# Optimization experiments

Hardware: AMD Instinct MI355X
Metric: run time of the kernel (lower is better)

Reference implementation:

```python
import jax, jax.numpy as jnp
import numpy as np

S, B, I, H, L, D = 512, 64, 128, 256, 6, 2  # seq, batch, input, hidden, layers, directions


def setup_inputs() -> dict:
    key = jax.random.key(0)
    ks = jax.random.split(key, 7)
    stdv = 1.0 / np.sqrt(H)
    u = lambda k, shape: jax.random.uniform(k, shape, jnp.float32, -stdv, stdv)
    return {
        "x": jax.random.normal(ks[0], (S, B, I), jnp.float32),
        "h0": jax.random.normal(ks[1], (L * D, B, H), jnp.float32),
        "w_ih0": u(ks[2], (D, 3 * H, I)),            # layer 0 input weights
        "w_ih": u(ks[3], (L - 1, D, 3 * H, D * H)),  # layers 1.. input weights
        "w_hh": u(ks[4], (L, D, 3 * H, H)),
        "b_ih": u(ks[5], (L, D, 3 * H)),
        "b_hh": u(ks[6], (L, D, 3 * H)),
    }


def _gru_direction(gate_x, w_hh, b_hh, h0, reverse):
    # gate_x: (S, B, 3H) precomputed x @ W_ih.T + b_ih; scan the recurrence.
    def step(h, gx):
        gh = h @ w_hh.T + b_hh  # (B, 3H)
        x_r, x_z, x_n = jnp.split(gx, 3, axis=-1)
        h_r, h_z, h_n = jnp.split(gh, 3, axis=-1)
        r = jax.nn.sigmoid(x_r + h_r)
        z = jax.nn.sigmoid(x_z + h_z)
        n = jnp.tanh(x_n + r * h_n)
        h_new = (1.0 - z) * n + z * h
        return h_new, h_new

    h_last, ys = jax.lax.scan(step, h0, gate_x, reverse=reverse)
    return h_last, ys  # ys aligned with input time order even when reverse=True


def reference(x, h0, w_ih0, w_ih, w_hh, b_ih, b_hh):
    num_layers = w_hh.shape[0]
    inp = x  # (S, B, in_dim)
    h_n = []
    for layer in range(num_layers):
        outs = []
        for d in range(2):
            w = w_ih0[d] if layer == 0 else w_ih[layer - 1, d]
            # Single GEMM over the whole sequence for the input gates.
            gate_x = jnp.einsum('sbi,gi->sbg', inp, w) + b_ih[layer, d]
            h_last, ys = _gru_direction(
                gate_x, w_hh[layer, d], b_hh[layer, d],
                h0[layer * 2 + d], reverse=(d == 1))
            outs.append(ys)
            h_n.append(h_last)
        inp = jnp.concatenate(outs, axis=-1)  # (S, B, 2H)
    return jnp.stack(h_n)  # (L*2, B, H)
```

## Files before the change

kernel.cpp:

```cpp
#include <hip/hip_runtime.h>
#include <stdint.h>

#define S_LEN 512
#define NB    64
#define HID   256
#define G3    768
#define SB    32768
#define NLAYER 6

typedef short bf16x8 __attribute__((ext_vector_type(8)));
typedef short bf16x4 __attribute__((ext_vector_type(4)));
typedef float floatx4 __attribute__((ext_vector_type(4)));
typedef unsigned short u16;
typedef unsigned int   u32;

__device__ __forceinline__ float bf2f(u16 v) {
  u32 u = ((u32)v) << 16;
  return __builtin_bit_cast(float, u);
}
__device__ __forceinline__ u16 f2bf(float f) {
  u32 u = __builtin_bit_cast(u32, f);
  u = (u + 0x7FFFu + ((u >> 16) & 1u)) >> 16;
  return (u16)u;
}
__device__ __forceinline__ float fsigmoid(float x) {
  return __builtin_amdgcn_rcpf(1.0f + __expf(-x));
}
__device__ __forceinline__ float ftanh(float x) {
  return 1.0f - 2.0f * __builtin_amdgcn_rcpf(1.0f + __expf(x + x));
}

__device__ __forceinline__ void lds_barrier() {
  asm volatile("s_waitcnt lgkmcnt(0)\n\ts_barrier" ::: "memory");
}

__global__ void detect_fp32(const u16* __restrict__ x, int n, int* flag) {
  __shared__ int tot;
  if (threadIdx.x == 0) tot = 0;
  __syncthreads();
  int c = 0;
  for (int i = threadIdx.x; i < n; i += blockDim.x) {
    u16 v = x[i];
    if (((v >> 7) & 0xFF) == 0xFF) ++c;
  }
  atomicAdd(&tot, c);
  __syncthreads();
  if (threadIdx.x == 0) *flag = (tot > 64) ? 1 : 0;
}

__global__ void cvt(const void* __restrict__ src, u16* __restrict__ dst,
                    int n, const int* __restrict__ flag) {
  const int stride = gridDim.x * blockDim.x;
  const bool isf32 = (*flag != 0);
  for (int i = blockIdx.x * blockDim.x + threadIdx.x; i < n; i += stride) {
    if (isf32) dst[i] = f2bf(((const float*)src)[i]);
    else       dst[i] = ((const u16*)src)[i];
  }
}

__global__ void prep_bias(const u16* __restrict__ bih, const u16* __restrict__ bhh,
                          float* __restrict__ bc, int n) {
  int i = blockIdx.x * blockDim.x + threadIdx.x;
  if (i >= n) return;
  int col = i % G3;
  float v = bf2f(bih[i]);
  if (col < 512) v += bf2f(bhh[i]);
  bc[i] = v;
}

__global__ void write_out(const float* __restrict__ hNs, void* __restrict__ out,
                          int n, const int* __restrict__ flag) {
  int i = blockIdx.x * blockDim.x + threadIdx.x;
  if (i >= n) return;
  if (*flag) ((float*)out)[i] = hNs[i];
  else       ((u16*)out)[i]   = f2bf(hNs[i]);
}

__global__ __launch_bounds__(256)
void gate_gemm(const u16* __restrict__ A, const u16* __restrict__ W,
               const float* __restrict__ bias, u16* __restrict__ outg, int K) {
  const int m0  = blockIdx.x * 128;
  const int n0  = blockIdx.y * 128;
  const int dir = blockIdx.z;
  W    += (size_t)dir * G3 * K;
  bias += (size_t)dir * G3;
  outg += (size_t)dir * (size_t)SB * G3;

  __shared__ __align__(16) u16 lA[8192];
  __shared__ __align__(16) u16 lB[8192];

  const int tid  = threadIdx.x;
  const int lane = tid & 63;
  const int wv   = tid >> 6;
  const int wm   = wv & 1, wn = wv >> 1;
  const int l15  = lane & 15, quad = lane >> 4;

  floatx4 acc[4][4] = {};

  for (int k0 = 0; k0 < K; k0 += 64) {
    bf16x8 ra[4], rb[4];
#pragma unroll
    for (int i = 0; i < 4; ++i) {
      int c   = i * 256 + tid;
      int row = c >> 3;
      int kc  = (c & 7) ^ (row & 7);
      ra[i] = *(const bf16x8*)(A + (size_t)(m0 + row) * K + (k0 + kc * 8));
      rb[i] = *(const bf16x8*)(W + (size_t)(n0 + row) * K + (k0 + kc * 8));
    }
    __syncthreads();
#pragma unroll
    for (int i = 0; i < 4; ++i) {
      *(bf16x8*)(lA + (size_t)(i * 256 + tid) * 8) = ra[i];
      *(bf16x8*)(lB + (size_t)(i * 256 + tid) * 8) = rb[i];
    }
    __syncthreads();

#pragma unroll
    for (int kt = 0; kt < 2; ++kt) {
      bf16x8 af[4], bfr[4];
#pragma unroll
      for (int mt = 0; mt < 4; ++mt) {
        int row = wm * 64 + mt * 16 + l15;
        int ch  = row * 8 + ((kt * 4 + quad) ^ (row & 7));
        af[mt] = *(const bf16x8*)(lA + ch * 8);
      }
#pragma unroll
      for (int nt = 0; nt < 4; ++nt) {
        int row = wn * 64 + nt * 16 + l15;
        int ch  = row * 8 + ((kt * 4 + quad) ^ (row & 7));
        bfr[nt] = *(const bf16x8*)(lB + ch * 8);
      }
#pragma unroll
      for (int mt = 0; mt < 4; ++mt)
#pragma unroll
        for (int nt = 0; nt < 4; ++nt)
          acc[mt][nt] = __builtin_amdgcn_mfma_f32_16x16x32_bf16(
              af[mt], bfr[nt], acc[mt][nt], 0, 0, 0);
    }
  }

  const int sIdx = (m0 >> 6) + wm;
#pragma unroll
  for (int nt = 0; nt < 4; ++nt) {
    int n    = n0 + wn * 64 + nt * 16 + l15;
    int g    = n >> 8, jc = n & 255;
    float bv = bias[n];
#pragma unroll
    for (int mt = 0; mt < 4; ++mt) {
      bf16x4 pk;
#pragma unroll
      for (int r = 0; r < 4; ++r) pk[r] = (short)f2bf(acc[mt][nt][r] + bv);
      *(bf16x4*)(outg + ((((size_t)mt * 512 + sIdx) * 256 + jc) * 3 + g) * 16 +
                 quad * 4) = pk;
    }
  }
}

__global__ __launch_bounds__(512)
__attribute__((amdgpu_waves_per_eu(2, 2)))
void gru_scan(const u16* __restrict__ gateX,
              const u16* __restrict__ Whh,
              const u16* __restrict__ Bhh,
              const u16* __restrict__ H0,
              u16* __restrict__ layerOut,
              float* __restrict__ hNs,
              int layer) {
  const int dir = blockIdx.x & 1;
  const int bg  = blockIdx.x >> 1;
  const int tid = threadIdx.x;
  const int lane = tid & 63;
  const int wv   = tid >> 6;
  const int l15  = lane & 15, quad = lane >> 4;

  __shared__ __align__(16) u16 wnL[65536];
  __shared__ __align__(16) u16 hb2[2][4096];

  const u16* Wd = Whh + (size_t)dir * G3 * HID;

#pragma unroll
  for (int i = 0; i < 16; ++i) {
    int c    = i * 512 + tid;
    int n    = c >> 5;
    int slot = c & 31;
    bf16x8 v = *(const bf16x8*)(Wd + (size_t)(512 + n) * HID + slot * 8);
    *(bf16x8*)(wnL + n * 256 + ((slot ^ (n & 7)) * 8)) = v;
  }

  bf16x8 wrz[8][2][2];
#pragma unroll
  for (int g = 0; g < 2; ++g)
#pragma unroll
    for (int nt = 0; nt < 2; ++nt) {
      int n = g * 256 + wv * 32 + nt * 16 + l15;
#pragma unroll
      for (int kt = 0; kt < 8; ++kt)
        wrz[kt][g][nt] = *(const bf16x8*)(Wd + (size_t)n * HID + kt * 32 + quad * 8);
    }
#pragma unroll
  for (int kt = 0; kt < 8; ++kt)
#pragma unroll
    for (int g = 0; g < 2; ++g)
#pragma unroll
      for (int nt = 0; nt < 2; ++nt)
        asm volatile("" : "+v"(wrz[kt][g][nt]));

  float bhn[2];
#pragma unroll
  for (int nt = 0; nt < 2; ++nt)
    bhn[nt] = bf2f(Bhh[dir * G3 + 512 + wv * 32 + nt * 16 + l15]);

  const int mrow = quad * 4;
  const int b0   = bg * 16 + mrow;

  {
    int row = tid >> 5, slot = tid & 31;
    const u16* hp = H0 + ((size_t)(layer * 2 + dir) * NB + bg * 16 + row) * HID + slot * 8;
    *(bf16x8*)(&hb2[0][row * 256 + ((slot ^ (row & 7)) * 8)]) = *(const bf16x8*)hp;
  }
  float hreg[2][4];
#pragma unroll
  for (int nt = 0; nt < 2; ++nt)
#pragma unroll
    for (int r = 0; r < 4; ++r)
      hreg[nt][r] = bf2f(H0[((size_t)(layer * 2 + dir) * NB + b0 + r) * HID +
                            wv * 32 + nt * 16 + l15]);

  const long sstep = dir ? -(long)(256 * 3 * 16) : (long)(256 * 3 * 16);
  const u16* xb;
  {
    const int s0 = dir ? (S_LEN - 1) : 0;
    xb = gateX + (size_t)dir * SB * G3 +
         ((((size_t)bg * 512 + s0) * 256 + (wv * 32 + l15)) * 3) * 16 + quad * 4;
  }
  bf16x4 xp[3][2];
#pragma unroll
  for (int g = 0; g < 3; ++g)
#pragma unroll
    for (int nt = 0; nt < 2; ++nt)
      xp[g][nt] = *(const bf16x4*)(xb + nt * 768 + g * 16);
  xb += sstep;

  lds_barrier();

  for (int t = 0; t < S_LEN; ++t) {
    const int cur = t & 1, nxt = cur ^ 1;

    floatx4 aR[2], aZ[2], aN[2];
    float xnf[2][4];
#pragma unroll
    for (int nt = 0; nt < 2; ++nt)
#pragma unroll
      for (int r = 0; r < 4; ++r) {
        aR[nt][r]  = bf2f((u16)xp[0][nt][r]);
        aZ[nt][r]  = bf2f((u16)xp[1][nt][r]);
        xnf[nt][r] = bf2f((u16)xp[2][nt][r]);
        aN[nt][r]  = bhn[nt];
      }

#pragma unroll
    for (int g = 0; g < 3; ++g)
#pragma unroll
      for (int nt = 0; nt < 2; ++nt)
        xp[g][nt] = *(const bf16x4*)(xb + nt * 768 + g * 16);
    xb += sstep;

    if (t > 0) {
      const int sPrev = dir ? (S_LEN - t) : (t - 1);
      int row = tid >> 5, slot = tid & 31;
      bf16x8 hv = *(const bf16x8*)(&hb2[cur][row * 256 + ((slot ^ (row & 7)) * 8)]);
      *(bf16x8*)(layerOut + ((size_t)sPrev * NB + bg * 16 + row) * 512 +
                 dir * HID + slot * 8) = hv;
    }

#pragma unroll
    for (int kt = 0; kt < 8; ++kt) {
      const int sl = ((kt * 4 + quad) ^ (l15 & 7)) * 8;
      bf16x8 af  = *(const bf16x8*)(&hb2[cur][l15 * 256 + sl]);
      bf16x8 bn0 = *(const bf16x8*)(wnL + (wv * 32 + l15) * 256 + sl);
      bf16x8 bn1 = *(const bf16x8*)(wnL + (wv * 32 + 16 + l15) * 256 + sl);
      aR[0] = __builtin_amdgcn_mfma_f32_16x16x32_bf16(af, wrz[kt][0][0], aR[0], 0, 0, 0);
      aR[1] = __builtin_amdgcn_mfma_f32_16x16x32_bf16(af, wrz[kt][0][1], aR[1], 0, 0, 0);
      aZ[0] = __builtin_amdgcn_mfma_f32_16x16x32_bf16(af, wrz[kt][1][0], aZ[0], 0, 0, 0);
      aZ[1] = __builtin_amdgcn_mfma_f32_16x16x32_bf16(af, wrz[kt][1][1], aZ[1], 0, 0, 0);
      aN[0] = __builtin_amdgcn_mfma_f32_16x16x32_bf16(af, bn0,           aN[0], 0, 0, 0);
      aN[1] = __builtin_amdgcn_mfma_f32_16x16x32_bf16(af, bn1,           aN[1], 0, 0, 0);
    }

#pragma unroll
    for (int nt = 0; nt < 2; ++nt) {
      const int jc  = wv * 32 + nt * 16 + l15;
      const int jhi = jc >> 3, jlo = jc & 7;
#pragma unroll
      for (int r = 0; r < 4; ++r) {
        float rg = fsigmoid(aR[nt][r]);
        float zg = fsigmoid(aZ[nt][r]);
        float ng = ftanh(xnf[nt][r] + rg * aN[nt][r]);
        float hn = ng + zg * (hreg[nt][r] - ng);
        hreg[nt][r] = hn;
        int b = mrow + r;
        hb2[nxt][b * 256 + ((jhi ^ (b & 7)) * 8) + jlo] = f2bf(hn);
      }
    }

    lds_barrier();
  }

  {
    const int sLast = dir ? 0 : (S_LEN - 1);
    int row = tid >> 5, slot = tid & 31;
    bf16x8 hv = *(const bf16x8*)(&hb2[0][row * 256 + ((slot ^ (row & 7)) * 8)]);
    *(bf16x8*)(layerOut + ((size_t)sLast * NB + bg * 16 + row) * 512 +
               dir * HID + slot * 8) = hv;
  }
#pragma unroll
  for (int nt = 0; nt < 2; ++nt)
#pragma unroll
    for (int r = 0; r < 4; ++r)
      hNs[((size_t)(layer * 2 + dir) * NB + b0 + r) * HID +
          wv * 32 + nt * 16 + l15] = hreg[nt][r];
}

extern "C" void kernel_launch(void* const* d_in, const int* in_sizes, int n_in,
                              void* d_out, int out_size, void* d_ws, size_t ws_size,
                              hipStream_t stream) {
  (void)n_in; (void)ws_size;
  char* ws = (char*)d_ws;
  int*   flag  = (int*)ws;
  float* hNs   = (float*)(ws + 4096);
  float* biasC = (float*)(ws + 790528);
  u16*   h0C   = (u16*)(ws + (1u << 20));
  u16*   wih0C = h0C   + 196608;
  u16*   wihC  = wih0C + 196608;
  u16*   whhC  = wihC  + 3932160;
  u16*   bihC  = whhC  + 2359296;
  u16*   bhhC  = bihC  + 9216;
  u16*   gateX = (u16*)(ws + (16u  << 20));
  u16*   bufA  = (u16*)(ws + (112u << 20));
  u16*   bufB  = (u16*)(ws + (144u << 20));
  u16*   xC    = bufB;

  detect_fp32<<<1, 1024, 0, stream>>>((const u16*)d_in[0], 262144, flag);
  cvt<<<512, 256, 0, stream>>>(d_in[0], xC,    in_sizes[0], flag);
  cvt<<<256, 256, 0, stream>>>(d_in[1], h0C,   in_sizes[1], flag);
  cvt<<<256, 256, 0, stream>>>(d_in[2], wih0C, in_sizes[2], flag);
  cvt<<<512, 256, 0, stream>>>(d_in[3], wihC,  in_sizes[3], flag);
  cvt<<<512, 256, 0, stream>>>(d_in[4], whhC,  in_sizes[4], flag);
  cvt<<< 64, 256, 0, stream>>>(d_in[5], bihC,  in_sizes[5], flag);
  cvt<<< 64, 256, 0, stream>>>(d_in[6], bhhC,  in_sizes[6], flag);
  prep_bias<<<36, 256, 0, stream>>>(bihC, bhhC, biasC, NLAYER * 2 * G3);

  for (int layer = 0; layer < NLAYER; ++layer) {
    const u16* inp = (layer == 0) ? xC : ((layer & 1) ? bufA : bufB);
    u16* outBuf    = (layer & 1) ? bufB : bufA;

    const int K = (layer == 0) ? 128 : 512;
    const u16* W = (layer == 0) ? wih0C
                                : (wihC + (size_t)(layer - 1) * 2 * G3 * 512);
    dim3 grid(256, 6, 2);
    gate_gemm<<<grid, 256, 0, stream>>>(inp, W, biasC + (size_t)layer * 2 * G3,
                                        gateX, K);
    gru_scan<<<8, 512, 0, stream>>>(gateX, whhC + (size_t)layer * 2 * G3 * HID,
                                    bhhC + (size_t)layer * 2 * G3, h0C,
                                    outBuf, hNs, layer);
  }
  write_out<<<(out_size + 255) / 256, 256, 0, stream>>>(hNs, d_out, out_size, flag);
}
```

Baseline: 6.189 ms.

## Keep all recurrent weights in registers and read previous hidden state from LDS

The n-gate recurrent weights move from a 128KB LDS buffer into per-wave registers, so each step no longer issues two LDS weight reads per k-tile. The fp32 hidden-state registers are dropped; the previous h is re-read as bf16 from the LDS double buffer, results are packed with v_cvt_pk_bf16, and the output pointer advances incrementally. This raises register pressure and stores the recurrent state only at bf16 precision, which may increase accumulated rounding error. The final hidden output is now taken from the bf16 buffer.

After: 8.815 ms. 42.4% more time.

```diff
diff --git a/kernel.cpp b/kernel.cpp
--- a/kernel.cpp
+++ b/kernel.cpp
@@ -28,6 +28,11 @@
 }
 __device__ __forceinline__ float ftanh(float x) {
   return 1.0f - 2.0f * __builtin_amdgcn_rcpf(1.0f + __expf(x + x));
+}
+__device__ __forceinline__ u32 pk_bf16(float lo, float hi) {
+  u32 r;
+  asm("v_cvt_pk_bf16_f32 %0, %1, %2" : "=v"(r) : "v"(lo), "v"(hi));
+  return r;
 }
 
 __device__ __forceinline__ void lds_barrier() {
@@ -172,37 +177,27 @@
   const int wv   = tid >> 6;
   const int l15  = lane & 15, quad = lane >> 4;
 
-  __shared__ __align__(16) u16 wnL[65536];
   __shared__ __align__(16) u16 hb2[2][4096];
 
   const u16* Wd = Whh + (size_t)dir * G3 * HID;
 
-#pragma unroll
-  for (int i = 0; i < 16; ++i) {
-    int c    = i * 512 + tid;
-    int n    = c >> 5;
-    int slot = c & 31;
-    bf16x8 v = *(const bf16x8*)(Wd + (size_t)(512 + n) * HID + slot * 8);
-    *(bf16x8*)(wnL + n * 256 + ((slot ^ (n & 7)) * 8)) = v;
-  }
-
-  bf16x8 wrz[8][2][2];
-#pragma unroll
-  for (int g = 0; g < 2; ++g)
+  bf16x8 wfr[8][3][2];
+#pragma unroll
+  for (int g = 0; g < 3; ++g)
 #pragma unroll
     for (int nt = 0; nt < 2; ++nt) {
       int n = g * 256 + wv * 32 + nt * 16 + l15;
 #pragma unroll
       for (int kt = 0; kt < 8; ++kt)
-        wrz[kt][g][nt] = *(const bf16x8*)(Wd + (size_t)n * HID + kt * 32 + quad * 8);
+        wfr[kt][g][nt] = *(const bf16x8*)(Wd + (size_t)n * HID + kt * 32 + quad * 8);
     }
 #pragma unroll
   for (int kt = 0; kt < 8; ++kt)
 #pragma unroll
-    for (int g = 0; g < 2; ++g)
+    for (int g = 0; g < 3; ++g)
 #pragma unroll
       for (int nt = 0; nt < 2; ++nt)
-        asm volatile("" : "+v"(wrz[kt][g][nt]));
+        asm volatile("" : "+v"(wfr[kt][g][nt]));
 
   float bhn[2];
 #pragma unroll
@@ -210,20 +205,24 @@
     bhn[nt] = bf2f(Bhh[dir * G3 + 512 + wv * 32 + nt * 16 + l15]);
 
   const int mrow = quad * 4;
-  const int b0   = bg * 16 + mrow;
 
   {
     int row = tid >> 5, slot = tid & 31;
     const u16* hp = H0 + ((size_t)(layer * 2 + dir) * NB + bg * 16 + row) * HID + slot * 8;
     *(bf16x8*)(&hb2[0][row * 256 + ((slot ^ (row & 7)) * 8)]) = *(const bf16x8*)hp;
   }
-  float hreg[2][4];
-#pragma unroll
-  for (int nt = 0; nt < 2; ++nt)
-#pragma unroll
-    for (int r = 0; r < 4; ++r)
-      hreg[nt][r] = bf2f(H0[((size_t)(layer * 2 + dir) * NB + b0 + r) * HID +
-                            wv * 32 + nt * 16 + l15]);
+
+  int haddr[2][4];
+#pragma unroll
+  for (int nt = 0; nt < 2; ++nt) {
+    const int jc  = wv * 32 + nt * 16 + l15;
+    const int jhi = jc >> 3, jlo = jc & 7;
+#pragma unroll
+    for (int r = 0; r < 4; ++r) {
+      const int b = mrow + r;
+      haddr[nt][r] = b * 256 + ((jhi ^ (b & 7)) * 8) + jlo;
+    }
+  }
 
   const long sstep = dir ? -(long)(256 * 3 * 16) : (long)(256 * 3 * 16);
   const u16* xb;
@@ -240,21 +239,29 @@
       xp[g][nt] = *(const bf16x4*)(xb + nt * 768 + g * 16);
   xb += sstep;
 
+  u16* loPtr;
+  {
+    int row = tid >> 5, slot = tid & 31;
+    const int sFirst = dir ? (S_LEN - 1) : 0;
+    loPtr = layerOut + ((size_t)sFirst * NB + bg * 16 + row) * 512 +
+            dir * HID + slot * 8;
+  }
+  const long lostep = dir ? -(long)(NB * 512) : (long)(NB * 512);
+
   lds_barrier();
 
   for (int t = 0; t < S_LEN; ++t) {
     const int cur = t & 1, nxt = cur ^ 1;
 
     floatx4 aR[2], aZ[2], aN[2];
-    float xnf[2][4];
+    bf16x4 xn0 = xp[2][0], xn1 = xp[2][1];
 #pragma unroll
     for (int nt = 0; nt < 2; ++nt)
 #pragma unroll
       for (int r = 0; r < 4; ++r) {
-        aR[nt][r]  = bf2f((u16)xp[0][nt][r]);
-        aZ[nt][r]  = bf2f((u16)xp[1][nt][r]);
-        xnf[nt][r] = bf2f((u16)xp[2][nt][r]);
-        aN[nt][r]  = bhn[nt];
+        aR[nt][r] = bf2f((u16)xp[0][nt][r]);
+        aZ[nt][r] = bf2f((u16)xp[1][nt][r]);
+        aN[nt][r] = bhn[nt];
       }
 
 #pragma unroll
@@ -262,62 +269,72 @@
 #pragma unroll
       for (int nt = 0; nt < 2; ++nt)
         xp[g][nt] = *(const bf16x4*)(xb + nt * 768 + g * 16);
-    xb += sstep;
+    if (t < S_LEN - 1) xb += sstep;
+
+    u16 hp[2][4];
+#pragma unroll
+    for (int nt = 0; nt < 2; ++nt)
+#pragma unroll
+      for (int r = 0; r < 4; ++r)
+        hp[nt][r] = hb2[cur][haddr[nt][r]];
 
     if (t > 0) {
-      const int sPrev = dir ? (S_LEN - t) : (t - 1);
       int row = tid >> 5, slot = tid & 31;
       bf16x8 hv = *(const bf16x8*)(&hb2[cur][row * 256 + ((slot ^ (row & 7)) * 8)]);
-      *(bf16x8*)(layerOut + ((size_t)sPrev * NB + bg * 16 + row) * 512 +
-                 dir * HID + slot * 8) = hv;
+      *(bf16x8*)loPtr = hv;
+      loPtr += lostep;
     }
 
 #pragma unroll
     for (int kt = 0; kt < 8; ++kt) {
       const int sl = ((kt * 4 + quad) ^ (l15 & 7)) * 8;
-      bf16x8 af  = *(const bf16x8*)(&hb2[cur][l15 * 256 + sl]);
-      bf16x8 bn0 = *(const bf16x8*)(wnL + (wv * 32 + l15) * 256 + sl);
-      bf16x8 bn1 = *(const bf16x8*)(wnL + (wv * 32 + 16 + l15) * 256 + sl);
-      aR[0] = __builtin_amdgcn_mfma_f32_16x16x32_bf16(af, wrz[kt][0][0], aR[0], 0, 0, 0);
-      aR[1] = __builtin_amdgcn_mfma_f32_16x16x32_bf16(af, wrz[kt][0][1], aR[1], 0, 0, 0);
-      aZ[0] = __builtin_amdgcn_mfma_f32_16x16x32_bf16(af, wrz[kt][1][0], aZ[0], 0, 0, 0);
-      aZ[1] = __builtin_amdgcn_mfma_f32_16x16x32_bf16(af, wrz[kt][1][1], aZ[1], 0, 0, 0);
-      aN[0] = __builtin_amdgcn_mfma_f32_16x16x32_bf16(af, bn0,           aN[0], 0, 0, 0);
-      aN[1] = __builtin_amdgcn_mfma_f32_16x16x32_bf16(af, bn1,           aN[1], 0, 0, 0);
+      bf16x8 af = *(const bf16x8*)(&hb2[cur][l15 * 256 + sl]);
+      aR[0] = __builtin_amdgcn_mfma_f32_16x16x32_bf16(af, wfr[kt][0][0], aR[0], 0, 0, 0);
+      aR[1] = __builtin_amdgcn_mfma_f32_16x16x32_bf16(af, wfr[kt][0][1], aR[1], 0, 0, 0);
+      aZ[0] = __builtin_amdgcn_mfma_f32_16x16x32_bf16(af, wfr[kt][1][0], aZ[0], 0, 0, 0);
+      aZ[1] = __builtin_amdgcn_mfma_f32_16x16x32_bf16(af, wfr[kt][1][1], aZ[1], 0, 0, 0);
+      aN[0] = __builtin_amdgcn_mfma_f32_16x16x32_bf16(af, wfr[kt][2][0], aN[0], 0, 0, 0);
+      aN[1] = __builtin_amdgcn_mfma_f32_16x16x32_bf16(af, wfr[kt][2][1], aN[1], 0, 0, 0);
     }
 
 #pragma unroll
     for (int nt = 0; nt < 2; ++nt) {
-      const int jc  = wv * 32 + nt * 16 + l15;
-      const int jhi = jc >> 3, jlo = jc & 7;
+      const bf16x4 xn = nt ? xn1 : xn0;
+      float hn[4];
 #pragma unroll
       for (int r = 0; r < 4; ++r) {
         float rg = fsigmoid(aR[nt][r]);
         float zg = fsigmoid(aZ[nt][r]);
-        float ng = ftanh(xnf[nt][r] + rg * aN[nt][r]);
-        float hn = ng + zg * (hreg[nt][r] - ng);
-        hreg[nt][r] = hn;
-        int b = mrow + r;
-        hb2[nxt][b * 256 + ((jhi ^ (b & 7)) * 8) + jlo] = f2bf(hn);
+        float ng = ftanh(bf2f((u16)xn[r]) + rg * aN[nt][r]);
+        float h0 = bf2f(hp[nt][r]);
+        hn[r] = ng + zg * (h0 - ng);
       }
+      u32 p01 = pk_bf16(hn[0], hn[1]);
+      u32 p23 = pk_bf16(hn[2], hn[3]);
+      hb2[nxt][haddr[nt][0]] = (u16)p01;
+      hb2[nxt][haddr[nt][1]] = (u16)(p01 >> 16);
+      hb2[nxt][haddr[nt][2]] = (u16)p23;
+      hb2[nxt][haddr[nt][3]] = (u16)(p23 >> 16);
     }
 
     lds_barrier();
   }
 
   {
+    int row = tid >> 5, slot = tid & 31;
     const int sLast = dir ? 0 : (S_LEN - 1);
-    int row = tid >> 5, slot = tid & 31;
     bf16x8 hv = *(const bf16x8*)(&hb2[0][row * 256 + ((slot ^ (row & 7)) * 8)]);
     *(bf16x8*)(layerOut + ((size_t)sLast * NB + bg * 16 + row) * 512 +
                dir * HID + slot * 8) = hv;
-  }
-#pragma unroll
-  for (int nt = 0; nt < 2; ++nt)
-#pragma unroll
-    for (int r = 0; r < 4; ++r)
-      hNs[((size_t)(layer * 2 + dir) * NB + b0 + r) * HID +
-          wv * 32 + nt * 16 + l15] = hreg[nt][r];
+    float* dst = hNs + ((size_t)(layer * 2 + dir) * NB + bg * 16 + row) * HID + slot * 8;
+    floatx4 v0, v1;
+#pragma unroll
+    for (int i = 0; i < 4; ++i) v0[i] = bf2f((u16)hv[i]);
+#pragma unroll
+    for (int i = 0; i < 4; ++i) v1[i] = bf2f((u16)hv[4 + i]);
+    *(floatx4*)dst = v0;
+    *((floatx4*)dst + 1) = v1;
+  }
 }
 
 extern "C" void kernel_launch(void* const* d_in, const int* in_sizes, int n_in,
```
